# Optimization experiments

Hardware: AMD Instinct MI355X
Metric: run time of the kernel (lower is better)

The kernel has to match this reference:

```python
import jax, jax.numpy as jnp
import numpy as np
from jax import lax

EPS = 1e-5

def conv2d(x, w, b, pad):
    y = lax.conv_general_dilated(x, w, (1, 1), [(pad, pad), (pad, pad)],
                                 dimension_numbers=('NCHW', 'OIHW', 'NCHW'))
    return y + b[None, :, None, None]

def batchnorm(x, gamma, beta):
    mean = jnp.mean(x, axis=(0, 2, 3), keepdims=True)
    var = jnp.var(x, axis=(0, 2, 3), keepdims=True)  # biased, as torch BN training mode
    return gamma[None, :, None, None] * (x - mean) * lax.rsqrt(var + EPS) + beta[None, :, None, None]

def maxpool2(x):
    return lax.reduce_window(x, -jnp.inf, lax.max, (1, 1, 2, 2), (1, 1, 2, 2), 'VALID')

def upsample(x, s):
    N, C, H, W = x.shape
    return jax.image.resize(x, (N, C, H * s, W * s), method='bilinear')

def select_topvar(x, k=3):
    # per-sample, per-channel unbiased variance; gather top-k variance channels
    N, C, H, W = x.shape
    v = jnp.var(x.reshape(N, C, H * W), axis=-1, ddof=1)  # [N, C]
    _, idx = lax.top_k(v, k)                              # argsort(-v)[:k]
    return jnp.take_along_axis(x, idx[:, :, None, None], axis=1)

def setup_inputs() -> dict:
    key = jax.random.key(0)
    ks = jax.random.split(key, 16)
    n_channel, n_class = 10, 5
    d = {}
    d['x'] = jax.random.normal(ks[0], (16, n_channel, 512, 512), jnp.float32)
    sc = 0.1
    d['w_ext1'] = jax.random.normal(ks[1], (16, n_channel, 1, 1), jnp.float32) * sc
    d['b_ext1'] = jnp.zeros((16,), jnp.float32)
    d['g_ebn1'] = jnp.ones((16,), jnp.float32)
    d['be_ebn1'] = jnp.zeros((16,), jnp.float32)
    d['w_ext2'] = jax.random.normal(ks[2], (16, 16, 1, 1), jnp.float32) * sc
    d['b_ext2'] = jnp.zeros((16,), jnp.float32)
    d['g_ebn2'] = jnp.ones((16,), jnp.float32)
    d['be_ebn2'] = jnp.zeros((16,), jnp.float32)
    d['w_c1'] = jax.random.normal(ks[3], (8, 3, 3, 3), jnp.float32) * sc
    d['b_c1'] = jnp.zeros((8,), jnp.float32)
    d['w_c2'] = jax.random.normal(ks[4], (16, 8, 3, 3), jnp.float32) * sc
    d['b_c2'] = jnp.zeros((16,), jnp.float32)
    d['g_bn1'] = jnp.ones((16,), jnp.float32)
    d['be_bn1'] = jnp.zeros((16,), jnp.float32)
    d['g_bn2'] = jnp.ones((8,), jnp.float32)
    d['be_bn2'] = jnp.zeros((8,), jnp.float32)
    d['w_1k'] = jax.random.normal(ks[5], (n_class, 24, 1, 1), jnp.float32) * sc
    d['b_1k'] = jnp.zeros((n_class,), jnp.float32)
    return d

def reference(x, w_ext1, b_ext1, g_ebn1, be_ebn1, w_ext2, b_ext2, g_ebn2, be_ebn2,
              w_c1, b_c1, w_c2, b_c2, g_bn1, be_bn1, g_bn2, be_bn2, w_1k, b_1k):
    # bandExtract: 1x1 conv -> BN -> sigmoid, twice
    h = jax.nn.sigmoid(batchnorm(conv2d(x, w_ext1, b_ext1, 0), g_ebn1, be_ebn1))
    h = jax.nn.sigmoid(batchnorm(conv2d(h, w_ext2, b_ext2, 0), g_ebn2, be_ebn2))
    # featureSelect: keep 3 channels with largest per-sample variance
    x0 = select_topvar(h, 3)                                   # [N,3,H,W]
    x1 = maxpool2(jax.nn.sigmoid(conv2d(x0, w_c1, b_c1, 1)))   # [N,8,H/2,W/2]
    x2 = maxpool2(jax.nn.sigmoid(conv2d(x1, w_c2, b_c2, 1)))   # [N,16,H/4,W/4]
    x2 = batchnorm(jax.nn.relu(upsample(x2, 4)), g_bn1, be_bn1)  # [N,16,H,W]
    x1 = batchnorm(jax.nn.relu(upsample(x1, 2)), g_bn2, be_bn2)  # [N,8,H,W]
    merge = jnp.concatenate([x1, x2], axis=1)                    # [N,24,H,W]
    return conv2d(merge, w_1k, b_1k, 0)                          # [N,n_class,H,W]
```

## Files before the change

### kernel.cpp

```cpp
#include <hip/hip_runtime.h>
#include <math.h>

#define N_    16
#define CIN_  10
#define CB_   16
#define H_    512
#define W_    512
#define HW_   (512*512)
#define EPSF  1e-5f

__device__ __forceinline__ float sgm(float z){
  float e = __builtin_amdgcn_exp2f(z * -1.44269504088896f);
  return __builtin_amdgcn_rcpf(1.0f + e);
}

__global__ void k_zero(double* __restrict__ p, int n){
  int i = blockIdx.x*256 + threadIdx.x;
  if (i < n) p[i] = 0.0;
}

__global__ void k_fin(const double* __restrict__ S, const float* __restrict__ g,
                      const float* __restrict__ be, float* __restrict__ AB,
                      int C, double invM){
  int c = threadIdx.x;
  if (c < C){
    double s=0.0,q=0.0;
    for (int n=0;n<N_;++n){ s+=S[(n*C+c)*2]; q+=S[(n*C+c)*2+1]; }
    double mean = s*invM;
    double var  = q*invM - mean*mean;
    float a = g[c]*rsqrtf((float)var + EPSF);
    AB[c]   = a;
    AB[C+c] = be[c] - (float)mean*a;
  }
}

__global__ __launch_bounds__(256) void k_cov(
    const float* __restrict__ x, double* __restrict__ SP)
{
  const int n = blockIdx.y;
  const int base = blockIdx.x*4096;
  const float* xp = x + (size_t)n*CIN_*HW_;
  float s[CIN_], p[55];
#pragma unroll
  for (int i=0;i<CIN_;++i) s[i]=0.f;
#pragma unroll
  for (int i=0;i<55;++i) p[i]=0.f;
#pragma unroll 1
  for (int it=0; it<4; ++it){
    const int off = base + it*1024 + threadIdx.x*4;
    float4 xv[CIN_];
#pragma unroll
    for (int ci=0; ci<CIN_; ++ci)
      xv[ci] = *(const float4*)(xp + (size_t)ci*HW_ + off);
#pragma unroll
    for (int ci=0; ci<CIN_; ++ci)
      s[ci] += xv[ci].x + xv[ci].y + xv[ci].z + xv[ci].w;
    int k=0;
#pragma unroll
    for (int i=0;i<CIN_;++i)
#pragma unroll
      for (int j=i;j<CIN_;++j,++k)
        p[k] += xv[i].x*xv[j].x + xv[i].y*xv[j].y + xv[i].z*xv[j].z + xv[i].w*xv[j].w;
  }
  __shared__ float red[4][65];
  const int lane = threadIdx.x & 63, wid = threadIdx.x >> 6;
#pragma unroll
  for (int k=0;k<65;++k){
    float v = (k<CIN_) ? s[k] : p[k-CIN_];
    for (int o=32;o>0;o>>=1) v += __shfl_down(v,o);
    if (lane==0) red[wid][k]=v;
  }
  __syncthreads();
  if (threadIdx.x < 65){
    float v = red[0][threadIdx.x]+red[1][threadIdx.x]+red[2][threadIdx.x]+red[3][threadIdx.x];
    atomicAdd(&SP[n*65+threadIdx.x], (double)v);
  }
}

__global__ void k_fin1(const double* __restrict__ SP, const float* __restrict__ w1,
                       const float* __restrict__ b1, const float* __restrict__ g,
                       const float* __restrict__ be, float* __restrict__ AB){
  __shared__ double Sm[CIN_], Cv[55];
  int t = threadIdx.x;
  if (t < 65){
    double s = 0.0;
    for (int n=0;n<N_;++n) s += SP[n*65+t];
    if (t < CIN_) Sm[t] = s; else Cv[t-CIN_] = s;
  }
  __syncthreads();
  if (t < CB_){
    const double M = 16.0*(double)HW_;
    double b = (double)b1[t];
    double wd[CIN_];
    double lin = 0.0;
    for (int i=0;i<CIN_;++i){ wd[i] = (double)w1[t*CIN_+i]; lin += wd[i]*Sm[i]/M; }
    double mean = b + lin;
    double ey2 = b*b + 2.0*b*lin;
    int k=0;
    for (int i=0;i<CIN_;++i)
      for (int j=i;j<CIN_;++j,++k)
        ey2 += (i==j ? 1.0 : 2.0) * wd[i]*wd[j]*(Cv[k]/M);
    double var = ey2 - mean*mean;
    float a = g[t]*rsqrtf((float)var + EPSF);
    AB[t] = a;
    AB[CB_+t] = be[t] - (float)mean*a;
  }
}

__global__ __launch_bounds__(256) void k_band2(
    const float* __restrict__ x,
    const float* __restrict__ w1, const float* __restrict__ b1, const float* __restrict__ AB1,
    const float* __restrict__ w2, const float* __restrict__ b2,
    float* __restrict__ B, double* __restrict__ S2)
{
  const int n = blockIdx.y;
  const int base = blockIdx.x*4096;
  const float* xp = x + (size_t)n*CIN_*HW_;
  float* bp = B + (size_t)n*CB_*HW_;
  float sum[CB_], sq[CB_];
#pragma unroll
  for (int c=0;c<CB_;++c){ sum[c]=0.f; sq[c]=0.f; }
#pragma unroll 1
  for (int it=0; it<4; ++it){
    const int p = base + it*1024 + threadIdx.x*4;
    float4 xv[CIN_];
#pragma unroll
    for (int ci=0; ci<CIN_; ++ci)
      xv[ci] = *(const float4*)(xp + (size_t)ci*HW_ + p);
    float4 s[CB_];
#pragma unroll
    for (int co=0; co<CB_; ++co){
      float bb = b1[co];
      float ox=bb, oy=bb, oz=bb, ow=bb;
#pragma unroll
      for (int ci=0; ci<CIN_; ++ci){
        float w = w1[co*CIN_+ci];
        ox += w*xv[ci].x; oy += w*xv[ci].y; oz += w*xv[ci].z; ow += w*xv[ci].w;
      }
      const float a = AB1[co], sh = AB1[CB_+co];
      s[co].x = sgm(a*ox+sh); s[co].y = sgm(a*oy+sh);
      s[co].z = sgm(a*oz+sh); s[co].w = sgm(a*ow+sh);
    }
#pragma unroll
    for (int co=0; co<CB_; ++co){
      float bb = b2[co];
      float ox=bb, oy=bb, oz=bb, ow=bb;
#pragma unroll
      for (int ci=0; ci<CB_; ++ci){
        float w = w2[co*CB_+ci];
        ox += w*s[ci].x; oy += w*s[ci].y; oz += w*s[ci].z; ow += w*s[ci].w;
      }
      float4 o; o.x=ox; o.y=oy; o.z=oz; o.w=ow;
      *(float4*)(bp + (size_t)co*HW_ + p) = o;
      sum[co] += ox+oy+oz+ow;
      sq[co]  += ox*ox+oy*oy+oz*oz+ow*ow;
    }
  }
  __shared__ float red[4][CB_][2];
  const int lane = threadIdx.x & 63, wid = threadIdx.x >> 6;
#pragma unroll
  for (int c=0;c<CB_;++c){
    float s=sum[c], q=sq[c];
    for (int off=32; off>0; off>>=1){ s += __shfl_down(s,off); q += __shfl_down(q,off); }
    if (lane==0){ red[wid][c][0]=s; red[wid][c][1]=q; }
  }
  __syncthreads();
  if (threadIdx.x < CB_*2){
    int c = threadIdx.x>>1, k = threadIdx.x&1;
    float t = red[0][c][k]+red[1][c][k]+red[2][c][k]+red[3][c][k];
    atomicAdd(&S2[(n*CB_+c)*2+k], (double)t);
  }
}

__global__ __launch_bounds__(256) void k_varstats(
    const float* __restrict__ B, const float* __restrict__ AB2, double* __restrict__ SV)
{
  const int n = blockIdx.z, c = blockIdx.y;
  const float a = AB2[c], b = AB2[CB_+c];
  const float* p = B + ((size_t)(n*CB_+c))*HW_ + blockIdx.x*4096;
  float sum=0.f, sq=0.f;
#pragma unroll 1
  for (int it=0; it<4; ++it){
    float4 v = *(const float4*)(p + it*1024 + threadIdx.x*4);
    v.x = sgm(a*v.x+b); v.y = sgm(a*v.y+b); v.z = sgm(a*v.z+b); v.w = sgm(a*v.w+b);
    sum += v.x+v.y+v.z+v.w;
    sq  += v.x*v.x+v.y*v.y+v.z*v.z+v.w*v.w;
  }
  __shared__ float red[4][2];
  const int lane = threadIdx.x & 63, wid = threadIdx.x >> 6;
  for (int off=32; off>0; off>>=1){ sum += __shfl_down(sum,off); sq += __shfl_down(sq,off); }
  if (lane==0){ red[wid][0]=sum; red[wid][1]=sq; }
  __syncthreads();
  if (threadIdx.x < 2){
    int k = threadIdx.x;
    float t = red[0][k]+red[1][k]+red[2][k]+red[3][k];
    atomicAdd(&SV[(n*CB_+c)*2+k], (double)t);
  }
}

__global__ void k_topk(const double* __restrict__ SV, int* __restrict__ IDX){
  __shared__ double var[N_][CB_];
  int t = threadIdx.x;
  if (t < N_*CB_){
    int n=t>>4, c=t&15;
    double s=SV[t*2], q=SV[t*2+1];
    const double M = (double)HW_;
    var[n][c] = (q - s*s/M)/(M-1.0);
  }
  __syncthreads();
  if (t < N_){
    double v[CB_];
#pragma unroll
    for (int c=0;c<CB_;++c) v[c]=var[t][c];
    for (int k=0;k<3;++k){
      int bi=0; double bv=v[0];
#pragma unroll
      for (int c=1;c<CB_;++c) if (v[c]>bv){ bv=v[c]; bi=c; }
      IDX[t*3+k]=bi; v[bi]=-1e300;
    }
  }
}

__global__ __launch_bounds__(256) void k_conv1p(
    const float* __restrict__ B, const int* __restrict__ IDX, const float* __restrict__ AB2,
    const float* __restrict__ w, const float* __restrict__ bias,
    float* __restrict__ X1)
{
  const int n = blockIdx.y, ho = blockIdx.x, wo = threadIdx.x;
  __shared__ float tile[3][4][516];
  __shared__ int chs[3];
  __shared__ float ca[3], cb[3];
  if (threadIdx.x < 3){
    int c = IDX[n*3+threadIdx.x];
    chs[threadIdx.x] = c;
    ca[threadIdx.x] = AB2[c];
    cb[threadIdx.x] = AB2[CB_+c];
  }
  __syncthreads();
#pragma unroll
  for (int k=0;k<3;++k){
    const float* pc = B + ((size_t)(n*CB_+chs[k]))*HW_;
    const float a = ca[k], bb = cb[k];
#pragma unroll
    for (int dy=0;dy<4;++dy){
      const int r = 2*ho-1+dy;
      float tx = 0.f, ty = 0.f;
      if (r>=0 && r<H_){
        const float2 v = *(const float2*)(pc + (size_t)r*W_ + 2*wo);
        tx = sgm(a*v.x+bb); ty = sgm(a*v.y+bb);
      }
      tile[k][dy][1+2*wo] = tx;
      tile[k][dy][2+2*wo] = ty;
    }
  }
  if (wo < 24){
    int k = wo>>3, dy = (wo&7)>>1;
    tile[k][dy][(wo&1) ? 513 : 0] = 0.f;
  }
  __syncthreads();
  float in[3][4][4];
#pragma unroll
  for (int k=0;k<3;++k)
#pragma unroll
    for (int dy=0;dy<4;++dy)
#pragma unroll
      for (int dx=0;dx<4;++dx)
        in[k][dy][dx] = tile[k][dy][2*wo+dx];
#pragma unroll
  for (int co=0;co<8;++co){
    float m = -1e30f;
#pragma unroll
    for (int py=0;py<2;++py)
#pragma unroll
    for (int px=0;px<2;++px){
      float acc = bias[co];
#pragma unroll
      for (int k=0;k<3;++k)
#pragma unroll
      for (int kh=0;kh<3;++kh)
#pragma unroll
      for (int kw=0;kw<3;++kw)
        acc += w[((co*3+k)*3+kh)*3+kw] * in[k][py+kh][px+kw];
      m = fmaxf(m, acc);
    }
    X1[((size_t)(n*8+co)*256 + ho)*256 + wo] = sgm(m);
  }
}

__global__ __launch_bounds__(256) void k_conv2p(
    const float* __restrict__ X1, const float* __restrict__ w, const float* __restrict__ bias,
    float* __restrict__ X2)
{
  const int n  = blockIdx.y;
  const int wo = threadIdx.x & 127;
  const int ho = blockIdx.x*2 + (threadIdx.x>>7);
  float acc[16][4];
#pragma unroll
  for (int co=0;co<16;++co){
    float bb = bias[co];
    acc[co][0]=bb; acc[co][1]=bb; acc[co][2]=bb; acc[co][3]=bb;
  }
#pragma unroll 1
  for (int ci=0; ci<8; ++ci){
    const float* p = X1 + ((size_t)(n*8+ci))*65536;
    float patch[4][4];
#pragma unroll
    for (int dy=0;dy<4;++dy){
      int r = 2*ho-1+dy;
      bool rok = (r>=0 && r<256);
#pragma unroll
      for (int dx=0;dx<4;++dx){
        int cc = 2*wo-1+dx;
        patch[dy][dx] = (rok && cc>=0 && cc<256) ? p[r*256+cc] : 0.f;
      }
    }
#pragma unroll
    for (int co=0;co<16;++co){
      const float* wp = w + (co*8+ci)*9;
#pragma unroll
      for (int py=0;py<2;++py)
#pragma unroll
      for (int px=0;px<2;++px){
        float a = acc[co][py*2+px];
#pragma unroll
        for (int kh=0;kh<3;++kh)
#pragma unroll
        for (int kw=0;kw<3;++kw)
          a += wp[kh*3+kw]*patch[py+kh][px+kw];
        acc[co][py*2+px] = a;
      }
    }
  }
#pragma unroll
  for (int co=0;co<16;++co){
    float m = fmaxf(fmaxf(acc[co][0],acc[co][1]), fmaxf(acc[co][2],acc[co][3]));
    X2[((size_t)(n*16+co)*128 + ho)*128 + wo] = sgm(m);
  }
}

__global__ __launch_bounds__(256) void k_stats_up4(
    const float* __restrict__ X2, double* __restrict__ SB1)
{
  const int n = blockIdx.z, c = blockIdx.y;
  const float* p = X2 + ((size_t)(n*16+c))*16384;
  const int id = blockIdx.x*256 + threadIdx.x;
  const int ho = id>>7, m = id&127;
  const int q = ho>>2, r = ho&3;
  int rA, rB; float wA;
  if (r==0){ rA=q-1; rB=q;   wA=0.375f; }
  else if (r==1){ rA=q-1; rB=q;   wA=0.125f; }
  else if (r==2){ rA=q;   rB=q+1; wA=0.875f; }
  else          { rA=q;   rB=q+1; wA=0.625f; }
  const float wB = 1.f-wA;
  rA = max(rA,0); rB = min(rB,127);
  const int c0 = max(m-1,0), c1 = m, c2 = min(m+1,127);
  const float* pa = p + rA*128; const float* pb = p + rB*128;
  float t0 = wA*pa[c0]+wB*pb[c0];
  float t1 = wA*pa[c1]+wB*pb[c1];
  float t2 = wA*pa[c2]+wB*pb[c2];
  float o0 = fmaxf(0.375f*t0+0.625f*t1, 0.f);
  float o1 = fmaxf(0.125f*t0+0.875f*t1, 0.f);
  float o2 = fmaxf(0.875f*t1+0.125f*t2, 0.f);
  float o3 = fmaxf(0.625f*t1+0.375f*t2, 0.f);
  float sum = o0+o1+o2+o3;
  float sq  = o0*o0+o1*o1+o2*o2+o3*o3;
  __shared__ float red[4][2];
  const int lane = threadIdx.x & 63, wid = threadIdx.x >> 6;
  for (int off=32; off>0; off>>=1){ sum += __shfl_down(sum,off); sq += __shfl_down(sq,off); }
  if (lane==0){ red[wid][0]=sum; red[wid][1]=sq; }
  __syncthreads();
  if (threadIdx.x < 2){
    int k = threadIdx.x;
    float t = red[0][k]+red[1][k]+red[2][k]+red[3][k];
    atomicAdd(&SB1[(n*16+c)*2+k], (double)t);
  }
}

__global__ __launch_bounds__(256) void k_stats_up2(
    const float* __restrict__ X1, double* __restrict__ SB2)
{
  const int n = blockIdx.z, c = blockIdx.y;
  const float* p = X1 + ((size_t)(n*8+c))*65536;
  const int id = blockIdx.x*256 + threadIdx.x;
  const int ho = id>>7, m = id&127;
  const int i = ho>>1, r = ho&1;
  int rA, rB; float wA;
  if (r==0){ rA=i-1; rB=i;   wA=0.25f; }
  else     { rA=i;   rB=i+1; wA=0.75f; }
  const float wB = 1.f-wA;
  rA = max(rA,0); rB = min(rB,255);
  const int c0 = max(2*m-1,0), c1 = 2*m, c2 = 2*m+1, c3 = min(2*m+2,255);
  const float* pa = p + rA*256; const float* pb = p + rB*256;
  float t0 = wA*pa[c0]+wB*pb[c0];
  float t1 = wA*pa[c1]+wB*pb[c1];
  float t2 = wA*pa[c2]+wB*pb[c2];
  float t3 = wA*pa[c3]+wB*pb[c3];
  float o0 = fmaxf(0.25f*t0+0.75f*t1, 0.f);
  float o1 = fmaxf(0.75f*t1+0.25f*t2, 0.f);
  float o2 = fmaxf(0.25f*t1+0.75f*t2, 0.f);
  float o3 = fmaxf(0.75f*t2+0.25f*t3, 0.f);
  float sum = o0+o1+o2+o3;
  float sq  = o0*o0+o1*o1+o2*o2+o3*o3;
  __shared__ float red[4][2];
  const int lane = threadIdx.x & 63, wid = threadIdx.x >> 6;
  for (int off=32; off>0; off>>=1){ sum += __shfl_down(sum,off); sq += __shfl_down(sq,off); }
  if (lane==0){ red[wid][0]=sum; red[wid][1]=sq; }
  __syncthreads();
  if (threadIdx.x < 2){
    int k = threadIdx.x;
    float t = red[0][k]+red[1][k]+red[2][k]+red[3][k];
    atomicAdd(&SB2[(n*8+c)*2+k], (double)t);
  }
}

__global__ __launch_bounds__(256) void k_final(
    const float* __restrict__ X1, const float* __restrict__ X2,
    const float* __restrict__ ABB1, const float* __restrict__ ABB2,
    const float* __restrict__ w1k, const float* __restrict__ b1k,
    float* __restrict__ out)
{
  const int n = blockIdx.y, bx = blockIdx.x, tid = threadIdx.x;
  __shared__ float sx1[8][3][256];
  __shared__ float sx2[16][2][128];
  {
    const int R0 = max(bx-1,0), R1 = bx, R2 = min(bx+1,255);
#pragma unroll
    for (int pr=0; pr<24; ++pr){
      const int ch = pr/3, row = pr%3;
      const int rr = (row==0) ? R0 : ((row==1) ? R1 : R2);
      sx1[ch][row][tid] = X1[((size_t)(n*8+ch)*256 + rr)*256 + tid];
    }
  }
  {
    const int q = bx>>1;
    const int Q0 = (bx&1) ? q : max(q-1,0);
    const int Q1 = (bx&1) ? min(q+1,127) : q;
    const int col = tid & 127, half = tid >> 7;
#pragma unroll
    for (int k=0;k<16;++k){
      const int pr = half + 2*k;
      const int ch = pr>>1, row = pr&1;
      const int rr = row ? Q1 : Q0;
      sx2[ch][row][col] = X2[((size_t)(n*16+ch)*128 + rr)*128 + col];
    }
  }
  __syncthreads();

  const int h = 2*bx + (tid>>7);
  const int m = tid & 127;
  float acc[5][4];
#pragma unroll
  for (int cls=0;cls<5;++cls){
    float bb = b1k[cls];
    acc[cls][0]=bb; acc[cls][1]=bb; acc[cls][2]=bb; acc[cls][3]=bb;
  }
  {
    const int r = h&1;
    const float wA = (r==0) ? 0.25f : 0.75f;
    const float wB = 1.f-wA;
    const int paL = r, pbL = r+1;
    const int c0 = max(2*m-1,0), c1 = 2*m, c2 = 2*m+1, c3 = min(2*m+2,255);
#pragma unroll
    for (int c=0;c<8;++c){
      const float* pa = &sx1[c][paL][0];
      const float* pb = &sx1[c][pbL][0];
      float t0 = wA*pa[c0]+wB*pb[c0];
      float t1 = wA*pa[c1]+wB*pb[c1];
      float t2 = wA*pa[c2]+wB*pb[c2];
      float t3 = wA*pa[c3]+wB*pb[c3];
      float o0 = 0.25f*t0+0.75f*t1, o1 = 0.75f*t1+0.25f*t2;
      float o2 = 0.25f*t1+0.75f*t2, o3 = 0.75f*t2+0.25f*t3;
      const float a = ABB2[c], bb = ABB2[8+c];
      o0 = a*fmaxf(o0,0.f)+bb; o1 = a*fmaxf(o1,0.f)+bb;
      o2 = a*fmaxf(o2,0.f)+bb; o3 = a*fmaxf(o3,0.f)+bb;
#pragma unroll
      for (int cls=0;cls<5;++cls){
        float wv = w1k[cls*24+c];
        acc[cls][0]+=wv*o0; acc[cls][1]+=wv*o1; acc[cls][2]+=wv*o2; acc[cls][3]+=wv*o3;
      }
    }
  }
  {
    const int r = h&3;
    float wA;
    if (r==0)      wA=0.375f;
    else if (r==1) wA=0.125f;
    else if (r==2) wA=0.875f;
    else           wA=0.625f;
    const float wB = 1.f-wA;
    const int c0 = max(m-1,0), c1 = m, c2 = min(m+1,127);
#pragma unroll
    for (int c=0;c<16;++c){
      const float* pa = &sx2[c][0][0];
      const float* pb = &sx2[c][1][0];
      float t0 = wA*pa[c0]+wB*pb[c0];
      float t1 = wA*pa[c1]+wB*pb[c1];
      float t2 = wA*pa[c2]+wB*pb[c2];
      float o0 = 0.375f*t0+0.625f*t1;
      float o1 = 0.125f*t0+0.875f*t1;
      float o2 = 0.875f*t1+0.125f*t2;
      float o3 = 0.625f*t1+0.375f*t2;
      const float a = ABB1[c], bb = ABB1[16+c];
      o0 = a*fmaxf(o0,0.f)+bb; o1 = a*fmaxf(o1,0.f)+bb;
      o2 = a*fmaxf(o2,0.f)+bb; o3 = a*fmaxf(o3,0.f)+bb;
#pragma unroll
      for (int cls=0;cls<5;++cls){
        float wv = w1k[cls*24+8+c];
        acc[cls][0]+=wv*o0; acc[cls][1]+=wv*o1; acc[cls][2]+=wv*o2; acc[cls][3]+=wv*o3;
      }
    }
  }
#pragma unroll
  for (int cls=0;cls<5;++cls){
    float4 v; v.x=acc[cls][0]; v.y=acc[cls][1]; v.z=acc[cls][2]; v.w=acc[cls][3];
    *(float4*)(out + ((size_t)(n*5+cls))*HW_ + (size_t)h*W_ + 4*m) = v;
  }
}

extern "C" void kernel_launch(void* const* d_in, const int* in_sizes, int n_in,
                              void* d_out, int out_size, void* d_ws, size_t ws_size,
                              hipStream_t stream) {
  const float* x       = (const float*)d_in[0];
  const float* w_ext1  = (const float*)d_in[1];
  const float* b_ext1  = (const float*)d_in[2];
  const float* g_ebn1  = (const float*)d_in[3];
  const float* be_ebn1 = (const float*)d_in[4];
  const float* w_ext2  = (const float*)d_in[5];
  const float* b_ext2  = (const float*)d_in[6];
  const float* g_ebn2  = (const float*)d_in[7];
  const float* be_ebn2 = (const float*)d_in[8];
  const float* w_c1    = (const float*)d_in[9];
  const float* b_c1    = (const float*)d_in[10];
  const float* w_c2    = (const float*)d_in[11];
  const float* b_c2    = (const float*)d_in[12];
  const float* g_bn1   = (const float*)d_in[13];
  const float* be_bn1  = (const float*)d_in[14];
  const float* g_bn2   = (const float*)d_in[15];
  const float* be_bn2  = (const float*)d_in[16];
  const float* w_1k    = (const float*)d_in[17];
  const float* b_1k    = (const float*)d_in[18];
  float* outp = (float*)d_out;

  char* ws = (char*)d_ws;
  float* B  = (float*)ws;
  float* X1 = (float*)(ws + 268435456);
  float* X2 = (float*)(ws + 268435456 + 33554432);
  char*  sb = ws + 268435456 + 33554432 + 16777216;
  double* SP  = (double*)sb;
  double* S2  = SP  + 1040;
  double* SV  = S2  + 512;
  double* SB1 = SV  + 512;
  double* SB2 = SB1 + 512;
  float*  AB1  = (float*)(SB2 + 256);
  float*  AB2  = AB1 + 32;
  float*  ABB1 = AB2 + 32;
  float*  ABB2 = ABB1 + 32;
  int*    IDX  = (int*)(ABB2 + 16);

  const double invM_bn = 1.0/4194304.0;

  k_zero<<<12,256,0,stream>>>(SP, 2832);
  k_cov<<<dim3(64,16),256,0,stream>>>(x, SP);
  k_fin1<<<1,128,0,stream>>>(SP, w_ext1, b_ext1, g_ebn1, be_ebn1, AB1);
  k_band2<<<dim3(64,16),256,0,stream>>>(x, w_ext1, b_ext1, AB1, w_ext2, b_ext2, B, S2);
  k_fin<<<1,64,0,stream>>>(S2, g_ebn2, be_ebn2, AB2, 16, invM_bn);
  k_varstats<<<dim3(64,16,16),256,0,stream>>>(B, AB2, SV);
  k_topk<<<1,256,0,stream>>>(SV, IDX);
  k_conv1p<<<dim3(256,16),256,0,stream>>>(B, IDX, AB2, w_c1, b_c1, X1);
  k_conv2p<<<dim3(64,16),256,0,stream>>>(X1, w_c2, b_c2, X2);
  k_stats_up4<<<dim3(256,16,16),256,0,stream>>>(X2, SB1);
  k_stats_up2<<<dim3(256,8,16),256,0,stream>>>(X1, SB2);
  k_fin<<<1,64,0,stream>>>(SB1, g_bn1, be_bn1, ABB1, 16, invM_bn);
  k_fin<<<1,64,0,stream>>>(SB2, g_bn2, be_bn2, ABB2, 8, invM_bn);
  k_final<<<dim3(256,16),256,0,stream>>>(X1, X2, ABB1, ABB2, w_1k, b_1k, outp);
}
```

Measured before the change: 800.3 us.

## Replace double atomics with per-block partials and fold BN1 into conv weights

The BN and variance statistics kernels now write per-block partial sums to scratch buffers instead of doing double-precision atomicAdds, and the finalize kernels reduce those partials. This removes the zeroing kernel and atomic contention. Two other changes ride along: the BN1 scale and shift are folded into the first 1x1 conv's weights and bias so k_band2 skips a per-element FMA, and the two upsample-stats kernels and their two finalize kernels are each merged into one launch. The catch is that k_fin1 now serially reduces 1024 partials per thread in a single block, and partial buffers alias workspace regions that are reused later.

```diff
diff --git a/kernel.cpp b/kernel.cpp
--- a/kernel.cpp
+++ b/kernel.cpp
@@ -14,28 +14,8 @@
   return __builtin_amdgcn_rcpf(1.0f + e);
 }
 
-__global__ void k_zero(double* __restrict__ p, int n){
-  int i = blockIdx.x*256 + threadIdx.x;
-  if (i < n) p[i] = 0.0;
-}
-
-__global__ void k_fin(const double* __restrict__ S, const float* __restrict__ g,
-                      const float* __restrict__ be, float* __restrict__ AB,
-                      int C, double invM){
-  int c = threadIdx.x;
-  if (c < C){
-    double s=0.0,q=0.0;
-    for (int n=0;n<N_;++n){ s+=S[(n*C+c)*2]; q+=S[(n*C+c)*2+1]; }
-    double mean = s*invM;
-    double var  = q*invM - mean*mean;
-    float a = g[c]*rsqrtf((float)var + EPSF);
-    AB[c]   = a;
-    AB[C+c] = be[c] - (float)mean*a;
-  }
-}
-
 __global__ __launch_bounds__(256) void k_cov(
-    const float* __restrict__ x, double* __restrict__ SP)
+    const float* __restrict__ x, double* __restrict__ SPp)
 {
   const int n = blockIdx.y;
   const int base = blockIdx.x*4096;
@@ -73,18 +53,19 @@
   __syncthreads();
   if (threadIdx.x < 65){
     float v = red[0][threadIdx.x]+red[1][threadIdx.x]+red[2][threadIdx.x]+red[3][threadIdx.x];
-    atomicAdd(&SP[n*65+threadIdx.x], (double)v);
-  }
-}
-
-__global__ void k_fin1(const double* __restrict__ SP, const float* __restrict__ w1,
+    SPp[((size_t)n*64 + blockIdx.x)*65 + threadIdx.x] = (double)v;
+  }
+}
+
+__global__ void k_fin1(const double* __restrict__ SPp, const float* __restrict__ w1,
                        const float* __restrict__ b1, const float* __restrict__ g,
-                       const float* __restrict__ be, float* __restrict__ AB){
+                       const float* __restrict__ be, float* __restrict__ AB,
+                       float* __restrict__ W1f, float* __restrict__ b1f){
   __shared__ double Sm[CIN_], Cv[55];
   int t = threadIdx.x;
   if (t < 65){
     double s = 0.0;
-    for (int n=0;n<N_;++n) s += SP[n*65+t];
+    for (int i=0;i<1024;++i) s += SPp[(size_t)i*65+t];
     if (t < CIN_) Sm[t] = s; else Cv[t-CIN_] = s;
   }
   __syncthreads();
@@ -102,16 +83,64 @@
         ey2 += (i==j ? 1.0 : 2.0) * wd[i]*wd[j]*(Cv[k]/M);
     double var = ey2 - mean*mean;
     float a = g[t]*rsqrtf((float)var + EPSF);
+    float sh = be[t] - (float)mean*a;
     AB[t] = a;
-    AB[CB_+t] = be[t] - (float)mean*a;
-  }
+    AB[CB_+t] = sh;
+    b1f[t] = a*b1[t] + sh;
+    for (int i=0;i<CIN_;++i) W1f[t*CIN_+i] = a*w1[t*CIN_+i];
+  }
+}
+
+template<int NB, int C>
+__device__ __forceinline__ void finp_body(
+    const double* __restrict__ P, const float* __restrict__ g,
+    const float* __restrict__ be, float* __restrict__ AB, double invM,
+    double* rs, double* rq)
+{
+  const int t = threadIdx.x;
+  const int c = t % C, slot = t / C, nslot = 256 / C;
+  const int tot = N_ * NB;
+  double s=0.0, q=0.0;
+  for (int j = slot; j < tot; j += nslot){
+    int n = j / NB, b = j - n*NB;
+    size_t idx = ((size_t)((n*C + c)*NB + b))*2;
+    s += P[idx]; q += P[idx+1];
+  }
+  rs[t]=s; rq[t]=q; __syncthreads();
+  for (int h = nslot>>1; h>0; h>>=1){
+    if (slot < h){ rs[t] += rs[t + h*C]; rq[t] += rq[t + h*C]; }
+    __syncthreads();
+  }
+  if (slot == 0){
+    double mean = rs[c]*invM;
+    double var  = rq[c]*invM - mean*mean;
+    float a = g[c]*rsqrtf((float)var + EPSF);
+    AB[c]   = a;
+    AB[C+c] = be[c] - (float)mean*a;
+  }
+}
+
+template<int NB, int C>
+__global__ void k_finp(const double* __restrict__ P, const float* __restrict__ g,
+                       const float* __restrict__ be, float* __restrict__ AB, double invM){
+  __shared__ double rs[256], rq[256];
+  finp_body<NB,C>(P, g, be, AB, invM, rs, rq);
+}
+
+__global__ void k_finup(const double* __restrict__ P1, const float* __restrict__ g1,
+                        const float* __restrict__ be1, float* __restrict__ A1,
+                        const double* __restrict__ P2, const float* __restrict__ g2,
+                        const float* __restrict__ be2, float* __restrict__ A2, double invM){
+  __shared__ double rs[256], rq[256];
+  if (blockIdx.x == 0) finp_body<256,16>(P1, g1, be1, A1, invM, rs, rq);
+  else                 finp_body<256,8 >(P2, g2, be2, A2, invM, rs, rq);
 }
 
 __global__ __launch_bounds__(256) void k_band2(
     const float* __restrict__ x,
-    const float* __restrict__ w1, const float* __restrict__ b1, const float* __restrict__ AB1,
+    const float* __restrict__ W1f, const float* __restrict__ b1f,
     const float* __restrict__ w2, const float* __restrict__ b2,
-    float* __restrict__ B, double* __restrict__ S2)
+    float* __restrict__ B, double* __restrict__ S2p)
 {
   const int n = blockIdx.y;
   const int base = blockIdx.x*4096;
@@ -130,16 +159,15 @@
     float4 s[CB_];
 #pragma unroll
     for (int co=0; co<CB_; ++co){
-      float bb = b1[co];
+      float bb = b1f[co];
       float ox=bb, oy=bb, oz=bb, ow=bb;
 #pragma unroll
       for (int ci=0; ci<CIN_; ++ci){
-        float w = w1[co*CIN_+ci];
+        float w = W1f[co*CIN_+ci];
         ox += w*xv[ci].x; oy += w*xv[ci].y; oz += w*xv[ci].z; ow += w*xv[ci].w;
       }
-      const float a = AB1[co], sh = AB1[CB_+co];
-      s[co].x = sgm(a*ox+sh); s[co].y = sgm(a*oy+sh);
-      s[co].z = sgm(a*oz+sh); s[co].w = sgm(a*ow+sh);
+      s[co].x = sgm(ox); s[co].y = sgm(oy);
+      s[co].z = sgm(oz); s[co].w = sgm(ow);
     }
 #pragma unroll
     for (int co=0; co<CB_; ++co){
@@ -168,12 +196,12 @@
   if (threadIdx.x < CB_*2){
     int c = threadIdx.x>>1, k = threadIdx.x&1;
     float t = red[0][c][k]+red[1][c][k]+red[2][c][k]+red[3][c][k];
-    atomicAdd(&S2[(n*CB_+c)*2+k], (double)t);
+    S2p[(((size_t)n*CB_ + c)*64 + blockIdx.x)*2 + k] = (double)t;
   }
 }
 
 __global__ __launch_bounds__(256) void k_varstats(
-    const float* __restrict__ B, const float* __restrict__ AB2, double* __restrict__ SV)
+    const float* __restrict__ B, const float* __restrict__ AB2, double* __restrict__ SVp)
 {
   const int n = blockIdx.z, c = blockIdx.y;
   const float a = AB2[c], b = AB2[CB_+c];
@@ -194,18 +222,21 @@
   if (threadIdx.x < 2){
     int k = threadIdx.x;
     float t = red[0][k]+red[1][k]+red[2][k]+red[3][k];
-    atomicAdd(&SV[(n*CB_+c)*2+k], (double)t);
-  }
-}
-
-__global__ void k_topk(const double* __restrict__ SV, int* __restrict__ IDX){
+    SVp[(((size_t)n*CB_ + c)*64 + blockIdx.x)*2 + k] = (double)t;
+  }
+}
+
+__global__ void k_topk(const double* __restrict__ SVp, int* __restrict__ IDX){
   __shared__ double var[N_][CB_];
   int t = threadIdx.x;
   if (t < N_*CB_){
-    int n=t>>4, c=t&15;
-    double s=SV[t*2], q=SV[t*2+1];
+    double s=0.0, q=0.0;
+    for (int b=0;b<64;++b){
+      s += SVp[((size_t)t*64+b)*2];
+      q += SVp[((size_t)t*64+b)*2+1];
+    }
     const double M = (double)HW_;
-    var[n][c] = (q - s*s/M)/(M-1.0);
+    var[t>>4][t&15] = (q - s*s/M)/(M-1.0);
   }
   __syncthreads();
   if (t < N_){
@@ -338,32 +369,58 @@
   }
 }
 
-__global__ __launch_bounds__(256) void k_stats_up4(
-    const float* __restrict__ X2, double* __restrict__ SB1)
-{
-  const int n = blockIdx.z, c = blockIdx.y;
-  const float* p = X2 + ((size_t)(n*16+c))*16384;
+__global__ __launch_bounds__(256) void k_upstats(
+    const float* __restrict__ X2, const float* __restrict__ X1,
+    double* __restrict__ SB1p, double* __restrict__ SB2p)
+{
+  const int n = blockIdx.z, y = blockIdx.y;
   const int id = blockIdx.x*256 + threadIdx.x;
   const int ho = id>>7, m = id&127;
-  const int q = ho>>2, r = ho&3;
-  int rA, rB; float wA;
-  if (r==0){ rA=q-1; rB=q;   wA=0.375f; }
-  else if (r==1){ rA=q-1; rB=q;   wA=0.125f; }
-  else if (r==2){ rA=q;   rB=q+1; wA=0.875f; }
-  else          { rA=q;   rB=q+1; wA=0.625f; }
-  const float wB = 1.f-wA;
-  rA = max(rA,0); rB = min(rB,127);
-  const int c0 = max(m-1,0), c1 = m, c2 = min(m+1,127);
-  const float* pa = p + rA*128; const float* pb = p + rB*128;
-  float t0 = wA*pa[c0]+wB*pb[c0];
-  float t1 = wA*pa[c1]+wB*pb[c1];
-  float t2 = wA*pa[c2]+wB*pb[c2];
-  float o0 = fmaxf(0.375f*t0+0.625f*t1, 0.f);
-  float o1 = fmaxf(0.125f*t0+0.875f*t1, 0.f);
-  float o2 = fmaxf(0.875f*t1+0.125f*t2, 0.f);
-  float o3 = fmaxf(0.625f*t1+0.375f*t2, 0.f);
-  float sum = o0+o1+o2+o3;
-  float sq  = o0*o0+o1*o1+o2*o2+o3*o3;
+  float sum, sq;
+  if (y < 16){
+    const int c = y;
+    const float* p = X2 + ((size_t)(n*16+c))*16384;
+    const int q = ho>>2, r = ho&3;
+    int rA, rB; float wA;
+    if (r==0){ rA=q-1; rB=q;   wA=0.375f; }
+    else if (r==1){ rA=q-1; rB=q;   wA=0.125f; }
+    else if (r==2){ rA=q;   rB=q+1; wA=0.875f; }
+    else          { rA=q;   rB=q+1; wA=0.625f; }
+    const float wB = 1.f-wA;
+    rA = max(rA,0); rB = min(rB,127);
+    const int c0 = max(m-1,0), c1 = m, c2 = min(m+1,127);
+    const float* pa = p + rA*128; const float* pb = p + rB*128;
+    float t0 = wA*pa[c0]+wB*pb[c0];
+    float t1 = wA*pa[c1]+wB*pb[c1];
+    float t2 = wA*pa[c2]+wB*pb[c2];
+    float o0 = fmaxf(0.375f*t0+0.625f*t1, 0.f);
+    float o1 = fmaxf(0.125f*t0+0.875f*t1, 0.f);
+    float o2 = fmaxf(0.875f*t1+0.125f*t2, 0.f);
+    float o3 = fmaxf(0.625f*t1+0.375f*t2, 0.f);
+    sum = o0+o1+o2+o3;
+    sq  = o0*o0+o1*o1+o2*o2+o3*o3;
+  } else {
+    const int c = y-16;
+    const float* p = X1 + ((size_t)(n*8+c))*65536;
+    const int i = ho>>1, r = ho&1;
+    int rA, rB; float wA;
+    if (r==0){ rA=i-1; rB=i;   wA=0.25f; }
+    else     { rA=i;   rB=i+1; wA=0.75f; }
+    const float wB = 1.f-wA;
+    rA = max(rA,0); rB = min(rB,255);
+    const int c0 = max(2*m-1,0), c1 = 2*m, c2 = 2*m+1, c3 = min(2*m+2,255);
+    const float* pa = p + rA*256; const float* pb = p + rB*256;
+    float t0 = wA*pa[c0]+wB*pb[c0];
+    float t1 = wA*pa[c1]+wB*pb[c1];
+    float t2 = wA*pa[c2]+wB*pb[c2];
+    float t3 = wA*pa[c3]+wB*pb[c3];
+    float o0 = fmaxf(0.25f*t0+0.75f*t1, 0.f);
+    float o1 = fmaxf(0.75f*t1+0.25f*t2, 0.f);
+    float o2 = fmaxf(0.25f*t1+0.75f*t2, 0.f);
+    float o3 = fmaxf(0.75f*t2+0.25f*t3, 0.f);
+    sum = o0+o1+o2+o3;
+    sq  = o0*o0+o1*o1+o2*o2+o3*o3;
+  }
   __shared__ float red[4][2];
   const int lane = threadIdx.x & 63, wid = threadIdx.x >> 6;
   for (int off=32; off>0; off>>=1){ sum += __shfl_down(sum,off); sq += __shfl_down(sq,off); }
@@ -372,44 +429,8 @@
   if (threadIdx.x < 2){
     int k = threadIdx.x;
     float t = red[0][k]+red[1][k]+red[2][k]+red[3][k];
-    atomicAdd(&SB1[(n*16+c)*2+k], (double)t);
-  }
-}
-
-__global__ __launch_bounds__(256) void k_stats_up2(
-    const float* __restrict__ X1, double* __restrict__ SB2)
-{
-  const int n = blockIdx.z, c = blockIdx.y;
-  const float* p = X1 + ((size_t)(n*8+c))*65536;
-  const int id = blockIdx.x*256 + threadIdx.x;
-  const int ho = id>>7, m = id&127;
-  const int i = ho>>1, r = ho&1;
-  int rA, rB; float wA;
-  if (r==0){ rA=i-1; rB=i;   wA=0.25f; }
-  else     { rA=i;   rB=i+1; wA=0.75f; }
-  const float wB = 1.f-wA;
-  rA = max(rA,0); rB = min(rB,255);
-  const int c0 = max(2*m-1,0), c1 = 2*m, c2 = 2*m+1, c3 = min(2*m+2,255);
-  const float* pa = p + rA*256; const float* pb = p + rB*256;
-  float t0 = wA*pa[c0]+wB*pb[c0];
-  float t1 = wA*pa[c1]+wB*pb[c1];
-  float t2 = wA*pa[c2]+wB*pb[c2];
-  float t3 = wA*pa[c3]+wB*pb[c3];
-  float o0 = fmaxf(0.25f*t0+0.75f*t1, 0.f);
-  float o1 = fmaxf(0.75f*t1+0.25f*t2, 0.f);
-  float o2 = fmaxf(0.25f*t1+0.75f*t2, 0.f);
-  float o3 = fmaxf(0.75f*t2+0.25f*t3, 0.f);
-  float sum = o0+o1+o2+o3;
-  float sq  = o0*o0+o1*o1+o2*o2+o3*o3;
-  __shared__ float red[4][2];
-  const int lane = threadIdx.x & 63, wid = threadIdx.x >> 6;
-  for (int off=32; off>0; off>>=1){ sum += __shfl_down(sum,off); sq += __shfl_down(sq,off); }
-  if (lane==0){ red[wid][0]=sum; red[wid][1]=sq; }
-  __syncthreads();
-  if (threadIdx.x < 2){
-    int k = threadIdx.x;
-    float t = red[0][k]+red[1][k]+red[2][k]+red[3][k];
-    atomicAdd(&SB2[(n*8+c)*2+k], (double)t);
+    if (y < 16) SB1p[(((size_t)n*16 + y)*256 + blockIdx.x)*2 + k] = (double)t;
+    else        SB2p[(((size_t)n*8 + (y-16))*256 + blockIdx.x)*2 + k] = (double)t;
   }
 }
 
@@ -545,32 +566,31 @@
   float* B  = (float*)ws;
   float* X1 = (float*)(ws + 268435456);
   float* X2 = (float*)(ws + 268435456 + 33554432);
+  double* SPp  = (double*)ws;
+  double* SB1p = (double*)ws;
+  double* SB2p = (double*)(ws + 1048576);
+  double* S2p  = (double*)(ws + 268435456);
+  double* SVp  = (double*)(ws + 268435456 + 262144);
   char*  sb = ws + 268435456 + 33554432 + 16777216;
-  double* SP  = (double*)sb;
-  double* S2  = SP  + 1040;
-  double* SV  = S2  + 512;
-  double* SB1 = SV  + 512;
-  double* SB2 = SB1 + 512;
-  float*  AB1  = (float*)(SB2 + 256);
+  float*  AB1  = (float*)sb;
   float*  AB2  = AB1 + 32;
   float*  ABB1 = AB2 + 32;
   float*  ABB2 = ABB1 + 32;
-  int*    IDX  = (int*)(ABB2 + 16);
+  float*  W1f  = ABB2 + 16;
+  float*  b1f  = W1f + 160;
+  int*    IDX  = (int*)(b1f + 16);
 
   const double invM_bn = 1.0/4194304.0;
 
-  k_zero<<<12,256,0,stream>>>(SP, 2832);
-  k_cov<<<dim3(64,16),256,0,stream>>>(x, SP);
-  k_fin1<<<1,128,0,stream>>>(SP, w_ext1, b_ext1, g_ebn1, be_ebn1, AB1);
-  k_band2<<<dim3(64,16),256,0,stream>>>(x, w_ext1, b_ext1, AB1, w_ext2, b_ext2, B, S2);
-  k_fin<<<1,64,0,stream>>>(S2, g_ebn2, be_ebn2, AB2, 16, invM_bn);
-  k_varstats<<<dim3(64,16,16),256,0,stream>>>(B, AB2, SV);
-  k_topk<<<1,256,0,stream>>>(SV, IDX);
+  k_cov<<<dim3(64,16),256,0,stream>>>(x, SPp);
+  k_fin1<<<1,128,0,stream>>>(SPp, w_ext1, b_ext1, g_ebn1, be_ebn1, AB1, W1f, b1f);
+  k_band2<<<dim3(64,16),256,0,stream>>>(x, W1f, b1f, w_ext2, b_ext2, B, S2p);
+  k_finp<64,16><<<1,256,0,stream>>>(S2p, g_ebn2, be_ebn2, AB2, invM_bn);
+  k_varstats<<<dim3(64,16,16),256,0,stream>>>(B, AB2, SVp);
+  k_topk<<<1,256,0,stream>>>(SVp, IDX);
   k_conv1p<<<dim3(256,16),256,0,stream>>>(B, IDX, AB2, w_c1, b_c1, X1);
   k_conv2p<<<dim3(64,16),256,0,stream>>>(X1, w_c2, b_c2, X2);
-  k_stats_up4<<<dim3(256,16,16),256,0,stream>>>(X2, SB1);
-  k_stats_up2<<<dim3(256,8,16),256,0,stream>>>(X1, SB2);
-  k_fin<<<1,64,0,stream>>>(SB1, g_bn1, be_bn1, ABB1, 16, invM_bn);
-  k_fin<<<1,64,0,stream>>>(SB2, g_bn2, be_bn2, ABB2, 8, invM_bn);
+  k_upstats<<<dim3(256,24,16),256,0,stream>>>(X2, X1, SB1p, SB2p);
+  k_finup<<<2,256,0,stream>>>(SB1p, g_bn1, be_bn1, ABB1, SB2p, g_bn2, be_bn2, ABB2, invM_bn);
   k_final<<<dim3(256,16),256,0,stream>>>(X1, X2, ABB1, ABB2, w_1k, b_1k, outp);
 }
```

New measurement: 824.2 us. 3.0% more time.
